# Performance work log

Hardware: AMD Instinct MI355X
Metric: run time of the kernel (lower is better)

Reference implementation:

```python
import jax, jax.numpy as jnp
import numpy as np

B, IN, OUT, ORDER = 8192, 1024, 1024, 7


def setup_inputs() -> dict:
    key = jax.random.key(0)
    k1, k2 = jax.random.split(key)
    x = jax.random.normal(k1, (B, IN), dtype=jnp.float32)
    tanh_range = jnp.float32(1.0)
    coef = jax.random.normal(k2, (OUT, IN, ORDER + 1), dtype=jnp.float32) * 0.1
    return {"x": x, "tanh_range": tanh_range, "coef": coef}


def _poly(x, tanh_range, order):
    # t^0, t^1, ..., t^order via cumulative products (matches torch recurrence)
    t = jnp.tanh(x * tanh_range)                      # [B, IN]
    powers = jnp.cumprod(jnp.broadcast_to(t[..., None], t.shape + (order,)), axis=-1)
    ones = jnp.ones_like(t)[..., None]
    return jnp.concatenate([ones, powers], axis=-1)   # [B, IN, order+1]


def reference(x, tanh_range, coef):
    poly = _poly(x, tanh_range, ORDER)                # [B, IN, K]
    # output[b, j] = sum_{i,k} coef[j,i,k] * poly[b,i,k]
    return jnp.einsum('bik,jik->bj', poly, coef)
```

## Files before the change

### kernel.cpp

```cpp
#include <hip/hip_runtime.h>
#include <hip/hip_bf16.h>


#define KT 7168
#define KFULL 8192

#define TM 128
#define TN 128
#define TK 64
#define NT (KT / TK)

#define BM 128
#define BN 128

typedef short bf16x8 __attribute__((ext_vector_type(8)));
typedef short bf16x4 __attribute__((ext_vector_type(4)));
typedef float f32x4  __attribute__((ext_vector_type(4)));

__device__ __forceinline__ unsigned short f2bf(float f) {
    union { float f; unsigned u; } v; v.f = f;
    unsigned r = v.u + 0x7fffu + ((v.u >> 16) & 1u);
    return (unsigned short)(r >> 16);
}

__device__ __forceinline__ void gload_lds16(const void* gp, void* lp) {
    __builtin_amdgcn_global_load_lds(
        (const __attribute__((address_space(1))) void*)gp,
        (__attribute__((address_space(3))) void*)lp, 16, 0, 0);
}

#define CVT_BLOCKS  512
#define TANH_BLOCKS 4096

__global__ __launch_bounds__(256)
void prep(const float* __restrict__ x, const float* __restrict__ trp,
          const float* __restrict__ coef, unsigned short* __restrict__ coef_bf,
          unsigned short* __restrict__ A, float* __restrict__ bias) {
    __shared__ float redbuf[4];

    const int t   = threadIdx.x;
    const int blk = blockIdx.x;
    const int rl  = t >> 7;
    const int ig  = t & 127;

    if (blk < CVT_BLOCKS) {
        const int j = blk * 2 + rl;
        const float* src = coef + (size_t)j * KFULL + ig * 64;
        float k0sum = 0.f;
        bf16x8 pl[7];
        #pragma unroll
        for (int i = 0; i < 8; ++i) {
            const float4 f0 = *(const float4*)(src + i * 8);
            const float4 f1 = *(const float4*)(src + i * 8 + 4);
            k0sum += f0.x;
            pl[0][i] = (short)f2bf(f0.y); pl[1][i] = (short)f2bf(f0.z);
            pl[2][i] = (short)f2bf(f0.w); pl[3][i] = (short)f2bf(f1.x);
            pl[4][i] = (short)f2bf(f1.y); pl[5][i] = (short)f2bf(f1.z);
            pl[6][i] = (short)f2bf(f1.w);
        }
        #pragma unroll
        for (int off = 32; off > 0; off >>= 1) k0sum += __shfl_down(k0sum, off, 64);
        if ((t & 63) == 0) redbuf[t >> 6] = k0sum;
        __syncthreads();
        if (t == 0)   bias[j]     = redbuf[0] + redbuf[1];
        if (t == 128) bias[j]     = redbuf[2] + redbuf[3];

        unsigned short* dst = coef_bf + (size_t)j * KT + ig * 8;
        #pragma unroll
        for (int p = 0; p < 7; ++p)
            *(bf16x8*)(dst + p * 1024) = pl[p];
    } else {
        const int bb = (blk - CVT_BLOCKS) * 2 + rl;
        const float tr = trp[0];
        const float* xp = x + (size_t)bb * 1024 + ig * 8;
        const float4 x0 = *(const float4*)xp;
        const float4 x1 = *(const float4*)(xp + 4);
        const float xs[8] = {x0.x, x0.y, x0.z, x0.w, x1.x, x1.y, x1.z, x1.w};
        bf16x8 pl[7];
        #pragma unroll
        for (int i = 0; i < 8; ++i) {
            const float e  = __expf(2.0f * tr * xs[i]);
            const float tt = 1.0f - 2.0f * __builtin_amdgcn_rcpf(e + 1.0f);
            float pw = tt;
            #pragma unroll
            for (int p = 0; p < 7; ++p) { pl[p][i] = (short)f2bf(pw); pw *= tt; }
        }
        unsigned short* dst = A + (size_t)bb * KT + ig * 8;
        #pragma unroll
        for (int p = 0; p < 7; ++p)
            *(bf16x8*)(dst + p * 1024) = pl[p];
    }
}

__global__ __launch_bounds__(256, 2)
void gemm_bt(const unsigned short* __restrict__ A, const unsigned short* __restrict__ Bt,
             const float* __restrict__ bias, float* __restrict__ out)
{
    __shared__ unsigned short As[2][TM * TK];
    __shared__ unsigned short Bs[2][TN * TK];

    const int t    = threadIdx.x;
    const int m0   = blockIdx.x * TM;
    const int n0   = blockIdx.y * TN;
    const int w    = t >> 6;
    const int lane = t & 63;
    const int wm   = (w >> 1) * 64;
    const int wn   = (w & 1) * 64;
    const int lrow = lane & 15;
    const int lq   = lane >> 4;

    const int S = ((lq ^ (lane & 7)) << 3);

    const int srow = t >> 3;
    const int schk = (t & 7) ^ (srow & 7);
    const size_t aG = (size_t)(m0 + srow) * KT + schk * 8;
    const size_t bG = (size_t)(n0 + srow) * KT + schk * 8;
    const int wofs = w * 512;

    f32x4 acc[4][4];
    #pragma unroll
    for (int i = 0; i < 4; i++)
        #pragma unroll
        for (int j = 0; j < 4; j++)
            acc[i][j] = (f32x4){0.f, 0.f, 0.f, 0.f};

    #pragma unroll
    for (int r = 0; r < 4; ++r) {
        gload_lds16(A  + aG + (size_t)(r * 32) * KT, &As[0][r * 2048 + wofs]);
        gload_lds16(Bt + bG + (size_t)(r * 32) * KT, &Bs[0][r * 2048 + wofs]);
    }
    __syncthreads();

    for (int kt = 0; kt < NT; ++kt) {
        const int cur = kt & 1;

        if (kt + 1 < NT) {
            const size_t ko = (size_t)(kt + 1) * TK;
            #pragma unroll
            for (int r = 0; r < 4; ++r) {
                gload_lds16(A  + aG + (size_t)(r * 32) * KT + ko, &As[cur ^ 1][r * 2048 + wofs]);
                gload_lds16(Bt + bG + (size_t)(r * 32) * KT + ko, &Bs[cur ^ 1][r * 2048 + wofs]);
            }
        }

        const unsigned short* as = As[cur];
        const unsigned short* bs = Bs[cur];
        bf16x8 a[2][4], b[2][4];
        #pragma unroll
        for (int i = 0; i < 4; ++i) {
            const int ro = (wm + i * 16 + lrow) * TK + S;
            a[0][i] = *(const bf16x8*)&as[ro];
            a[1][i] = *(const bf16x8*)&as[ro ^ 32];
        }
        #pragma unroll
        for (int j = 0; j < 4; ++j) {
            const int ro = (wn + j * 16 + lrow) * TK + S;
            b[0][j] = *(const bf16x8*)&bs[ro];
            b[1][j] = *(const bf16x8*)&bs[ro ^ 32];
        }
        #pragma unroll
        for (int kk = 0; kk < 2; ++kk)
            #pragma unroll
            for (int i = 0; i < 4; ++i)
                #pragma unroll
                for (int j = 0; j < 4; ++j)
                    acc[i][j] = __builtin_amdgcn_mfma_f32_16x16x32_bf16(
                        a[kk][i], b[kk][j], acc[i][j], 0, 0, 0);

        __syncthreads();
    }

    const int crow = (lane >> 4) * 4;
    const int ccol = lane & 15;
    #pragma unroll
    for (int j = 0; j < 4; j++) {
        const int n = n0 + wn + j * 16 + ccol;
        const float bv = bias[n];
        #pragma unroll
        for (int i = 0; i < 4; i++) {
            const int m = m0 + wm + i * 16 + crow;
            #pragma unroll
            for (int r = 0; r < 4; ++r)
                out[(size_t)(m + r) * 1024 + n] = acc[i][j][r] + bv;
        }
    }
}

#define LDK 72
__global__ __launch_bounds__(256, 2)
void taylor_gemm(const float* __restrict__ x, const float* __restrict__ trp,
                 const float* __restrict__ coef, float* __restrict__ out)
{
    __shared__ unsigned short As[BM * LDK];
    __shared__ unsigned short Bs[BN * LDK];

    const int t  = threadIdx.x;
    const int m0 = blockIdx.x * BM;
    const int n0 = blockIdx.y * BN;
    const float tr = trp[0];

    const int w    = t >> 6;
    const int lane = t & 63;
    const int wm   = (w >> 1) * 64;
    const int wn   = (w & 1) * 64;
    const int lrow = lane & 15;
    const int kq   = (lane >> 4) * 8;

    f32x4 acc[4][4];
    #pragma unroll
    for (int i = 0; i < 4; i++)
        #pragma unroll
        for (int j = 0; j < 4; j++)
            acc[i][j] = (f32x4){0.f, 0.f, 0.f, 0.f};

    const int bcol  = t & 15;
    const int brow0 = t >> 4;
    const int acol  = t & 7;
    const int arow0 = t >> 3;

    for (int k0 = 0; k0 < KFULL; k0 += 64) {
        const int i0 = k0 >> 3;
        #pragma unroll
        for (int r = 0; r < 8; ++r) {
            const int row = brow0 + r * 16;
            const float4 v = *(const float4*)(coef + (size_t)(n0 + row) * KFULL + k0 + bcol * 4);
            bf16x4 pk;
            pk[0] = (short)f2bf(v.x); pk[1] = (short)f2bf(v.y);
            pk[2] = (short)f2bf(v.z); pk[3] = (short)f2bf(v.w);
            *(bf16x4*)&Bs[row * LDK + bcol * 4] = pk;
        }
        #pragma unroll
        for (int r = 0; r < 4; ++r) {
            const int row = arow0 + r * 32;
            const float xv = x[(size_t)(m0 + row) * 1024 + i0 + acol];
            const float e  = __expf(2.0f * tr * xv);
            const float tt = 1.0f - 2.0f / (e + 1.0f);
            bf16x8 pk;
            float p = 1.0f;
            #pragma unroll
            for (int k = 0; k < 8; ++k) { pk[k] = (short)f2bf(p); p *= tt; }
            *(bf16x8*)&As[row * LDK + acol * 8] = pk;
        }
        __syncthreads();
        #pragma unroll
        for (int kk = 0; kk < 64; kk += 32) {
            bf16x8 a[4], b[4];
            #pragma unroll
            for (int i = 0; i < 4; i++)
                a[i] = *(const bf16x8*)&As[(wm + i * 16 + lrow) * LDK + kk + kq];
            #pragma unroll
            for (int j = 0; j < 4; j++)
                b[j] = *(const bf16x8*)&Bs[(wn + j * 16 + lrow) * LDK + kk + kq];
            #pragma unroll
            for (int i = 0; i < 4; i++)
                #pragma unroll
                for (int j = 0; j < 4; j++)
                    acc[i][j] = __builtin_amdgcn_mfma_f32_16x16x32_bf16(a[i], b[j], acc[i][j], 0, 0, 0);
        }
        __syncthreads();
    }

    const int crow = (lane >> 4) * 4;
    const int ccol = lane & 15;
    #pragma unroll
    for (int i = 0; i < 4; i++) {
        #pragma unroll
        for (int j = 0; j < 4; j++) {
            const int m = m0 + wm + i * 16 + crow;
            const int n = n0 + wn + j * 16 + ccol;
            #pragma unroll
            for (int r = 0; r < 4; ++r)
                out[(size_t)(m + r) * 1024 + n] = acc[i][j][r];
        }
    }
}

extern "C" void kernel_launch(void* const* d_in, const int* in_sizes, int n_in,
                              void* d_out, int out_size, void* d_ws, size_t ws_size,
                              hipStream_t stream) {
    const float* x    = (const float*)d_in[0];
    const float* trp  = (const float*)d_in[1];
    const float* coef = (const float*)d_in[2];
    float* out = (float*)d_out;

    const size_t A_BYTES    = (size_t)8192 * KT * 2;
    const size_t COEF_BYTES = (size_t)1024 * KT * 2;
    const size_t BIAS_BYTES = 1024 * sizeof(float);

    if (ws_size >= A_BYTES + COEF_BYTES + BIAS_BYTES) {
        unsigned short* A_bf    = (unsigned short*)d_ws;
        unsigned short* coef_bf = (unsigned short*)((char*)d_ws + A_BYTES);
        float*          bias    = (float*)((char*)d_ws + A_BYTES + COEF_BYTES);

        prep<<<dim3(CVT_BLOCKS + TANH_BLOCKS), dim3(256), 0, stream>>>(
            x, trp, coef, coef_bf, A_bf, bias);
        gemm_bt<<<dim3(8192 / TM, 1024 / TN), dim3(256), 0, stream>>>(
            A_bf, coef_bf, bias, out);
    } else {
        taylor_gemm<<<dim3(8192 / BM, 1024 / BN), dim3(256), 0, stream>>>(x, trp, coef, out);
    }
}
```

Baseline: 239.1 us.

## Enlarge GEMM M-tile to 256 with 512-thread blocks and explicit barriers

Doubles the GEMM block tile along M to 256 rows and uses 8 waves per block, remapping the global-to-LDS load loops so each tile of B is reused across twice as many A rows. The per-iteration __syncthreads is replaced with an explicit vmcnt wait plus a raw s_barrier. The bf16 conversion now uses the HIP intrinsic instead of a manual round-to-nearest-even. The larger tile raises LDS use to about 96KB per block, so likely only one block fits per CU, trading occupancy for less global traffic.

```diff
diff --git a/kernel.cpp b/kernel.cpp
--- a/kernel.cpp
+++ b/kernel.cpp
@@ -5,7 +5,7 @@
 #define KT 7168
 #define KFULL 8192
 
-#define TM 128
+#define TM 256
 #define TN 128
 #define TK 64
 #define NT (KT / TK)
@@ -18,9 +18,9 @@
 typedef float f32x4  __attribute__((ext_vector_type(4)));
 
 __device__ __forceinline__ unsigned short f2bf(float f) {
-    union { float f; unsigned u; } v; v.f = f;
-    unsigned r = v.u + 0x7fffu + ((v.u >> 16) & 1u);
-    return (unsigned short)(r >> 16);
+    union { __hip_bfloat16 h; unsigned short u; } v;
+    v.h = __float2bfloat16(f);
+    return v.u;
 }
 
 __device__ __forceinline__ void gload_lds16(const void* gp, void* lp) {
@@ -28,6 +28,12 @@
         (const __attribute__((address_space(1))) void*)gp,
         (__attribute__((address_space(3))) void*)lp, 16, 0, 0);
 }
+
+#define BARRIER() do { \
+    asm volatile("" ::: "memory"); \
+    __builtin_amdgcn_s_barrier(); \
+    asm volatile("" ::: "memory"); \
+} while (0)
 
 #define CVT_BLOCKS  512
 #define TANH_BLOCKS 4096
@@ -62,8 +68,8 @@
         for (int off = 32; off > 0; off >>= 1) k0sum += __shfl_down(k0sum, off, 64);
         if ((t & 63) == 0) redbuf[t >> 6] = k0sum;
         __syncthreads();
-        if (t == 0)   bias[j]     = redbuf[0] + redbuf[1];
-        if (t == 128) bias[j]     = redbuf[2] + redbuf[3];
+        if (t == 0)   bias[j] = redbuf[0] + redbuf[1];
+        if (t == 128) bias[j] = redbuf[2] + redbuf[3];
 
         unsigned short* dst = coef_bf + (size_t)j * KT + ig * 8;
         #pragma unroll
@@ -92,7 +98,7 @@
     }
 }
 
-__global__ __launch_bounds__(256, 2)
+__global__ __launch_bounds__(512, 2)
 void gemm_bt(const unsigned short* __restrict__ A, const unsigned short* __restrict__ Bt,
              const float* __restrict__ bias, float* __restrict__ out)
 {
@@ -125,11 +131,13 @@
             acc[i][j] = (f32x4){0.f, 0.f, 0.f, 0.f};
 
     #pragma unroll
-    for (int r = 0; r < 4; ++r) {
-        gload_lds16(A  + aG + (size_t)(r * 32) * KT, &As[0][r * 2048 + wofs]);
-        gload_lds16(Bt + bG + (size_t)(r * 32) * KT, &Bs[0][r * 2048 + wofs]);
-    }
-    __syncthreads();
+    for (int r = 0; r < 4; ++r)
+        gload_lds16(A + aG + (size_t)(r * 64) * KT, &As[0][r * 4096 + wofs]);
+    #pragma unroll
+    for (int r = 0; r < 2; ++r)
+        gload_lds16(Bt + bG + (size_t)(r * 64) * KT, &Bs[0][r * 4096 + wofs]);
+    asm volatile("s_waitcnt vmcnt(0)" ::: "memory");
+    BARRIER();
 
     for (int kt = 0; kt < NT; ++kt) {
         const int cur = kt & 1;
@@ -137,10 +145,11 @@
         if (kt + 1 < NT) {
             const size_t ko = (size_t)(kt + 1) * TK;
             #pragma unroll
-            for (int r = 0; r < 4; ++r) {
-                gload_lds16(A  + aG + (size_t)(r * 32) * KT + ko, &As[cur ^ 1][r * 2048 + wofs]);
-                gload_lds16(Bt + bG + (size_t)(r * 32) * KT + ko, &Bs[cur ^ 1][r * 2048 + wofs]);
-            }
+            for (int r = 0; r < 4; ++r)
+                gload_lds16(A + aG + (size_t)(r * 64) * KT + ko, &As[cur ^ 1][r * 4096 + wofs]);
+            #pragma unroll
+            for (int r = 0; r < 2; ++r)
+                gload_lds16(Bt + bG + (size_t)(r * 64) * KT + ko, &Bs[cur ^ 1][r * 4096 + wofs]);
         }
 
         const unsigned short* as = As[cur];
@@ -167,7 +176,8 @@
                     acc[i][j] = __builtin_amdgcn_mfma_f32_16x16x32_bf16(
                         a[kk][i], b[kk][j], acc[i][j], 0, 0, 0);
 
-        __syncthreads();
+        asm volatile("s_waitcnt vmcnt(0)" ::: "memory");
+        BARRIER();
     }
 
     const int crow = (lane >> 4) * 4;
@@ -191,8 +201,8 @@
 void taylor_gemm(const float* __restrict__ x, const float* __restrict__ trp,
                  const float* __restrict__ coef, float* __restrict__ out)
 {
-    __shared__ unsigned short As[BM * LDK];
-    __shared__ unsigned short Bs[BN * LDK];
+    __shared__ unsigned short Afs[BM * LDK];
+    __shared__ unsigned short Bfs[BN * LDK];
 
     const int t  = threadIdx.x;
     const int m0 = blockIdx.x * BM;
@@ -227,7 +237,7 @@
             bf16x4 pk;
             pk[0] = (short)f2bf(v.x); pk[1] = (short)f2bf(v.y);
             pk[2] = (short)f2bf(v.z); pk[3] = (short)f2bf(v.w);
-            *(bf16x4*)&Bs[row * LDK + bcol * 4] = pk;
+            *(bf16x4*)&Bfs[row * LDK + bcol * 4] = pk;
         }
         #pragma unroll
         for (int r = 0; r < 4; ++r) {
@@ -239,7 +249,7 @@
             float p = 1.0f;
             #pragma unroll
             for (int k = 0; k < 8; ++k) { pk[k] = (short)f2bf(p); p *= tt; }
-            *(bf16x8*)&As[row * LDK + acol * 8] = pk;
+            *(bf16x8*)&Afs[row * LDK + acol * 8] = pk;
         }
         __syncthreads();
         #pragma unroll
@@ -247,10 +257,10 @@
             bf16x8 a[4], b[4];
             #pragma unroll
             for (int i = 0; i < 4; i++)
-                a[i] = *(const bf16x8*)&As[(wm + i * 16 + lrow) * LDK + kk + kq];
+                a[i] = *(const bf16x8*)&Afs[(wm + i * 16 + lrow) * LDK + kk + kq];
             #pragma unroll
             for (int j = 0; j < 4; j++)
-                b[j] = *(const bf16x8*)&Bs[(wn + j * 16 + lrow) * LDK + kk + kq];
+                b[j] = *(const bf16x8*)&Bfs[(wn + j * 16 + lrow) * LDK + kk + kq];
             #pragma unroll
             for (int i = 0; i < 4; i++)
                 #pragma unroll
@@ -294,7 +304,7 @@
 
         prep<<<dim3(CVT_BLOCKS + TANH_BLOCKS), dim3(256), 0, stream>>>(
             x, trp, coef, coef_bf, A_bf, bias);
-        gemm_bt<<<dim3(8192 / TM, 1024 / TN), dim3(256), 0, stream>>>(
+        gemm_bt<<<dim3(8192 / TM, 1024 / TN), dim3(512), 0, stream>>>(
             A_bf, coef_bf, bias, out);
     } else {
         taylor_gemm<<<dim3(8192 / BM, 1024 / BN), dim3(256), 0, stream>>>(x, trp, coef, out);
```

Result: slower. 287.9 us (+20.4%).
